# Performance work log

Hardware: AMD Instinct MI355X
Metric: run time of the kernel (lower is better)

## Reference

```python
import jax, jax.numpy as jnp
import numpy as np

# config matching init_kwargs
C = 256; G = 16; GC = C // G; K = 3; P = K * K
PAD = 1; STR = 1; DIL = 1; OFFSET_SCALE = 1.0
N, H, W = 8, 64, 64


def setup_inputs() -> dict:
    key = jax.random.key(0)
    ks = jax.random.split(key, 8)
    def rn(k, shape, sc):
        return jax.random.normal(k, shape, jnp.float32) * sc
    return {
        "x": jax.random.normal(ks[0], (N, H, W, C), jnp.float32),
        "dw_w": rn(ks[1], (C, 1, K, K), 0.1),          # depthwise conv weight (OIHW, groups=C)
        "dw_b": jnp.zeros((C,), jnp.float32),
        "ln_g": jnp.ones((C,), jnp.float32),
        "ln_b": jnp.zeros((C,), jnp.float32),
        "off_w": rn(ks[2], (G * P * 2, C), 0.01),      # offset head (small so offsets stay sane)
        "off_b": jnp.zeros((G * P * 2,), jnp.float32),
        "mask_w": rn(ks[3], (G * P, C), 0.01),
        "mask_b": jnp.zeros((G * P,), jnp.float32),
        "in_w": rn(ks[4], (C, C), 0.05),
        "in_b": jnp.zeros((C,), jnp.float32),
        "out_w": rn(ks[5], (C, C), 0.05),
        "out_b": jnp.zeros((C,), jnp.float32),
    }


def _layer_norm(x, g, b, eps=1e-6):
    m = x.mean(-1, keepdims=True)
    v = ((x - m) ** 2).mean(-1, keepdims=True)
    return (x - m) * jax.lax.rsqrt(v + eps) * g + b


def _grid_sample_bilinear(img, grid):
    # img: (B, Cc, Hh, Ww); grid: (B, L, P, 2) normalized to [-1, 1], (x, y) order.
    # Matches torch.grid_sample(mode='bilinear', padding_mode='zeros', align_corners=False).
    B, Cc, Hh, Ww = img.shape
    gx = (grid[..., 0] + 1.0) * (Ww * 0.5) - 0.5
    gy = (grid[..., 1] + 1.0) * (Hh * 0.5) - 0.5
    x0 = jnp.floor(gx); y0 = jnp.floor(gy)
    tx = gx - x0; ty = gy - y0
    img_f = img.reshape(B, Cc, Hh * Ww)
    def corner(xi, yi, w):
        valid = (xi >= 0) & (xi < Ww) & (yi >= 0) & (yi < Hh)
        idx = (jnp.clip(yi, 0, Hh - 1) * Ww + jnp.clip(xi, 0, Ww - 1)).astype(jnp.int32)
        v = jnp.take_along_axis(img_f, idx.reshape(B, 1, -1), axis=2)  # (B, Cc, L*P)
        return v * (w * valid).reshape(B, 1, -1)
    out = (corner(x0, y0, (1 - tx) * (1 - ty)) + corner(x0 + 1, y0, tx * (1 - ty))
           + corner(x0, y0 + 1, (1 - tx) * ty) + corner(x0 + 1, y0 + 1, tx * ty))
    return out.reshape(B, Cc, grid.shape[1], grid.shape[2])  # (B, Cc, L, P)


def _dcnv3_core(x, offset, mask):
    # x: (N,H,W,C) value features; offset: (N,H,W,G*P*2); mask: (N,H,W,G*P)
    xpad = jnp.pad(x, ((0, 0), (PAD, PAD), (PAD, PAD), (0, 0)))
    Hi, Wi = H + 2 * PAD, W + 2 * PAD
    Ho, Wo = H, W
    # reference points (centers of receptive field), normalized by padded size
    start = (DIL * (K - 1)) // 2 + 0.5
    ry = (start + jnp.arange(Ho, dtype=jnp.float32) * STR) / Hi
    rx = (start + jnp.arange(Wo, dtype=jnp.float32) * STR) / Wi
    ref = jnp.stack([jnp.broadcast_to(rx[None, :], (Ho, Wo)),
                     jnp.broadcast_to(ry[:, None], (Ho, Wo))], -1)  # (Ho,Wo,2) (x,y)
    # dilation grid, x-major flattening to match torch meshgrid('ij') ordering
    d = jnp.arange(K, dtype=jnp.float32) * DIL - (DIL * (K - 1)) // 2
    kgrid = jnp.stack([jnp.repeat(d, K) / Wi, jnp.tile(d, K) / Hi], -1)  # (P,2)
    off = offset.reshape(N, Ho, Wo, G, P, 2)
    norm = jnp.array([Wi, Hi], jnp.float32)
    loc = (ref[None, :, :, None, None, :]
           + kgrid[None, None, None, None, :, :] * OFFSET_SCALE
           + off * OFFSET_SCALE / norm)                      # (N,Ho,Wo,G,P,2)
    sg = (2.0 * loc - 1.0).reshape(N, Ho * Wo, G, P, 2)
    sg = sg.transpose(0, 2, 1, 3, 4).reshape(N * G, Ho * Wo, P, 2)
    val = xpad.reshape(N, Hi * Wi, G * GC).transpose(0, 2, 1).reshape(N * G, GC, Hi, Wi)
    samp = _grid_sample_bilinear(val, sg)                    # (N*G, GC, Ho*Wo, P)
    m = mask.reshape(N, Ho * Wo, G, P).transpose(0, 2, 1, 3).reshape(N * G, 1, Ho * Wo, P)
    out = (samp * m).sum(-1)                                 # (N*G, GC, Ho*Wo)
    return out.reshape(N, G * GC, Ho * Wo).transpose(0, 2, 1).reshape(N, Ho, Wo, C)


def reference(x, dw_w, dw_b, ln_g, ln_b, off_w, off_b, mask_w, mask_b, in_w, in_b, out_w, out_b):
    xp = x @ in_w.T + in_b                                   # input_proj (values)
    # depthwise conv -> LN (channels_last) -> exact GELU
    y = jax.lax.conv_general_dilated(
        x.transpose(0, 3, 1, 2), dw_w, (1, 1), ((PAD, PAD), (PAD, PAD)),
        feature_group_count=C, dimension_numbers=('NCHW', 'OIHW', 'NCHW'))
    y = y + dw_b[None, :, None, None]
    x1 = jax.nn.gelu(_layer_norm(y.transpose(0, 2, 3, 1), ln_g, ln_b), approximate=False)
    offset = x1 @ off_w.T + off_b                            # (N,H,W,G*P*2)
    mlogits = (x1 @ mask_w.T + mask_b).reshape(N, H, W, G, P)
    mask = jax.nn.softmax(mlogits, axis=-1).reshape(N, H, W, G * P)
    out = _dcnv3_core(xp, offset, mask)
    return out @ out_w.T + out_b
```

## Files before the change

### kernel.cpp

```cpp
#include <hip/hip_runtime.h>


#define LL 32768
#define CC 256
#define HSTR 448

typedef __bf16 bf16;
typedef __bf16 bf16x4 __attribute__((ext_vector_type(4)));
typedef __bf16 bf16x8 __attribute__((ext_vector_type(8)));
typedef float f32x4v __attribute__((ext_vector_type(4)));
typedef float f32x2 __attribute__((ext_vector_type(2)));

__device__ __forceinline__ void gload16(const bf16* g, const bf16* lds_base) {
    __builtin_amdgcn_global_load_lds(
        (const __attribute__((address_space(1))) void*)g,
        (__attribute__((address_space(3))) void*)lds_base, 16, 0, 0);
}

__global__ __launch_bounds__(256) void k_prep(
    const float* __restrict__ in_w, const float* __restrict__ off_w,
    const float* __restrict__ mask_w, const float* __restrict__ out_w,
    const float* __restrict__ dw_w, const float* __restrict__ off_b,
    const float* __restrict__ mask_b,
    bf16* __restrict__ in_h, bf16* __restrict__ hw_h,
    bf16* __restrict__ out_h,
    float* __restrict__ dwT, float* __restrict__ hbias) {
    int idx = blockIdx.x * 256 + threadIdx.x;
    if (idx < 60416) {
        const float* s; bf16* hi; int i;
        if (idx < 16384)      { s = in_w;   hi = in_h;          i = idx; }
        else if (idx < 34816) { s = off_w;  hi = hw_h;          i = idx - 16384; }
        else if (idx < 44032) { s = mask_w; hi = hw_h + 73728;  i = idx - 34816; }
        else                  { s = out_w;  hi = out_h;         i = idx - 44032; }
        float4 v = *(const float4*)(s + (size_t)i * 4);
        bf16x4 h;
        h[0] = (bf16)v.x; h[1] = (bf16)v.y; h[2] = (bf16)v.z; h[3] = (bf16)v.w;
        *(bf16x4*)(hi + (size_t)i * 4) = h;
    } else if (idx < 62720) {
        int e = idx - 60416;
        int c = e & 255, j = e >> 8;
        dwT[j * 256 + c] = dw_w[c * 9 + j];
    } else if (idx < 63232) {
        int e = idx - 62720;
        hbias[e] = (e < 288) ? off_b[e] : (e < 432 ? mask_b[e - 288] : 0.f);
    } else if (idx < 68352) {
        int e = idx - 63232;
        bf16x4 z = {(bf16)0.f, (bf16)0.f, (bf16)0.f, (bf16)0.f};
        *(bf16x4*)(hw_h + 110592 + (size_t)e * 4) = z;
    }
}

__global__ __launch_bounds__(256) void k_dwln(
    const float* __restrict__ x, const float* __restrict__ dwT,
    const float* __restrict__ dw_b, const float* __restrict__ ln_g,
    const float* __restrict__ ln_b, bf16* __restrict__ x1h,
    bf16* __restrict__ xb) {
    int t = threadIdx.x;
    int q = t >> 6, u = t & 63;
    int l = blockIdx.x * 4 + q;
    int w = l & 63, h = (l >> 6) & 63, n = l >> 12;
    int c0 = u * 4;

    float4 acc = *(const float4*)(dw_b + c0);
    float4 xc = {0.f, 0.f, 0.f, 0.f};
#pragma unroll
    for (int kh = 0; kh < 3; ++kh) {
        int hh = h + kh - 1;
        if (hh < 0 || hh >= 64) continue;
#pragma unroll
        for (int kw = 0; kw < 3; ++kw) {
            int ww = w + kw - 1;
            if (ww < 0 || ww >= 64) continue;
            float4 xv = *(const float4*)(x + (size_t)(((n * 64 + hh) * 64) + ww) * CC + c0);
            if (kh == 1 && kw == 1) xc = xv;
            float4 wv = *(const float4*)(dwT + (kh * 3 + kw) * 256 + c0);
            acc.x += xv.x * wv.x; acc.y += xv.y * wv.y;
            acc.z += xv.z * wv.z; acc.w += xv.w * wv.w;
        }
    }
    bf16x4 xcb;
    xcb[0] = (bf16)xc.x; xcb[1] = (bf16)xc.y;
    xcb[2] = (bf16)xc.z; xcb[3] = (bf16)xc.w;
    *(bf16x4*)(xb + (size_t)l * CC + c0) = xcb;

    float s = acc.x + acc.y + acc.z + acc.w;
    float ss = acc.x * acc.x + acc.y * acc.y + acc.z * acc.z + acc.w * acc.w;
#pragma unroll
    for (int d = 1; d < 64; d <<= 1) {
        s += __shfl_xor(s, d);
        ss += __shfl_xor(ss, d);
    }
    float mean = s * (1.0f / 256.0f);
    float var = ss * (1.0f / 256.0f) - mean * mean;
    float rstd = rsqrtf(var + 1e-6f);
    float4 gv = *(const float4*)(ln_g + c0);
    float4 bv = *(const float4*)(ln_b + c0);
    float xn0 = (acc.x - mean) * rstd * gv.x + bv.x;
    float xn1 = (acc.y - mean) * rstd * gv.y + bv.y;
    float xn2 = (acc.z - mean) * rstd * gv.z + bv.z;
    float xn3 = (acc.w - mean) * rstd * gv.w + bv.w;
    bf16x4 oh;
    oh[0] = (bf16)(0.5f * xn0 * (1.0f + erff(xn0 * 0.70710678118654752f)));
    oh[1] = (bf16)(0.5f * xn1 * (1.0f + erff(xn1 * 0.70710678118654752f)));
    oh[2] = (bf16)(0.5f * xn2 * (1.0f + erff(xn2 * 0.70710678118654752f)));
    oh[3] = (bf16)(0.5f * xn3 * (1.0f + erff(xn3 * 0.70710678118654752f)));
    *(bf16x4*)(x1h + (size_t)l * CC + c0) = oh;
}

__device__ __forceinline__ void gemm_core(
    const bf16* __restrict__ A, const bf16* __restrict__ Wh,
    const float* __restrict__ bias, bf16* __restrict__ Cbf,
    int Nout, int cstride, int mb, int nb) {
    int t = threadIdx.x, wave = t >> 6, lane = t & 63;
    int wm = wave & 1, wn = wave >> 1;
    int fm = lane & 15, fq = lane >> 4;

    __shared__ bf16 smem[24576];

    const bf16* gbase[4];
    int lofs[4];
#pragma unroll
    for (int j = 0; j < 4; ++j) {
        int seg = wave * 4 + j;
        int arr = seg >> 3;
        int row = (seg & 7) * 16 + (lane >> 2);
        int col = (lane & 3) * 8;
        gbase[j] = (arr == 0) ? (A + (size_t)(mb + row) * CC + col)
                              : (Wh + (size_t)(nb + row) * CC + col);
        lofs[j] = seg * 512;
    }

    f32x4v acc[4][4];
#pragma unroll
    for (int i = 0; i < 4; ++i)
#pragma unroll
        for (int j = 0; j < 4; ++j) acc[i][j] = (f32x4v){0.f, 0.f, 0.f, 0.f};

#pragma unroll
    for (int j = 0; j < 4; ++j) gload16(gbase[j], smem + lofs[j]);
#pragma unroll
    for (int j = 0; j < 4; ++j) gload16(gbase[j] + 32, smem + 8192 + lofs[j]);

#pragma unroll
    for (int kt = 0; kt < 8; ++kt) {
        if (kt < 7)
            asm volatile("s_waitcnt vmcnt(4)\n\ts_barrier" ::: "memory");
        else
            asm volatile("s_waitcnt vmcnt(0)\n\ts_barrier" ::: "memory");
        if (kt < 6) {
#pragma unroll
            for (int j = 0; j < 4; ++j)
                gload16(gbase[j] + (kt + 2) * 32,
                        smem + ((kt + 2) % 3) * 8192 + lofs[j]);
        }
        const bf16* buf = smem + (kt % 3) * 8192;
        bf16x8 af[4], bfh[4];
#pragma unroll
        for (int i = 0; i < 4; ++i)
            af[i] = *(const bf16x8*)&buf[(wm * 64 + i * 16 + fm) * 32 + fq * 8];
#pragma unroll
        for (int j = 0; j < 4; ++j)
            bfh[j] = *(const bf16x8*)&buf[4096 + (wn * 64 + j * 16 + fm) * 32 + fq * 8];
#pragma unroll
        for (int i = 0; i < 4; ++i)
#pragma unroll
            for (int j = 0; j < 4; ++j)
                acc[i][j] = __builtin_amdgcn_mfma_f32_16x16x32_bf16(
                    af[i], bfh[j], acc[i][j], 0, 0, 0);
    }

#pragma unroll
    for (int j = 0; j < 4; ++j) {
        int n_g = nb + wn * 64 + j * 16 + fm;
        if (n_g >= Nout) continue;
        float bv = bias[n_g];
#pragma unroll
        for (int i = 0; i < 4; ++i) {
            int m_g = mb + wm * 64 + i * 16 + fq * 4;
#pragma unroll
            for (int rg = 0; rg < 4; ++rg)
                Cbf[(size_t)(m_g + rg) * cstride + n_g] = (bf16)(acc[i][j][rg] + bv);
        }
    }
}

__global__ __launch_bounds__(256) void k_gemm_ih(
    const bf16* __restrict__ xb, const bf16* __restrict__ x1h,
    const bf16* __restrict__ in_h, const bf16* __restrict__ hw_h,
    const float* __restrict__ in_b, const float* __restrict__ hbias,
    bf16* __restrict__ xpb, bf16* __restrict__ headb) {
    int mb = blockIdx.x * 128;
    int y = blockIdx.y;
    const bf16 *A, *W;
    const float* bs;
    bf16* Cb;
    int Nout, cstride, nb;
    if (y < 2) { A = xb;  W = in_h; bs = in_b;  Cb = xpb;   Nout = 256; cstride = 256;  nb = y * 128; }
    else       { A = x1h; W = hw_h; bs = hbias; Cb = headb; Nout = 432; cstride = HSTR; nb = (y - 2) * 128; }
    gemm_core(A, W, bs, Cb, Nout, cstride, mb, nb);
}

__global__ __launch_bounds__(256) void k_gemm_out(
    const bf16* __restrict__ A, const bf16* __restrict__ Wh,
    const float* __restrict__ bias, float* __restrict__ C32) {
    int mb = blockIdx.x * 64, nb = blockIdx.y * 128;
    int t = threadIdx.x, wave = t >> 6, lane = t & 63;
    int wm = wave & 1, wn = wave >> 1;
    int fm = lane & 15, fq = lane >> 4;

    __shared__ bf16 smem[18432];

    const bf16* gbase[3];
    int lofs[3];
#pragma unroll
    for (int j = 0; j < 3; ++j) {
        int seg = wave * 3 + j;
        int r16 = (seg < 4) ? seg : (seg - 4);
        int row = r16 * 16 + (lane >> 2);
        int col = (lane & 3) * 8;
        gbase[j] = (seg < 4) ? (A + (size_t)(mb + row) * CC + col)
                             : (Wh + (size_t)(nb + row) * CC + col);
        lofs[j] = seg * 512;
    }

    f32x4v acc[2][4];
#pragma unroll
    for (int i = 0; i < 2; ++i)
#pragma unroll
        for (int j = 0; j < 4; ++j) acc[i][j] = (f32x4v){0.f, 0.f, 0.f, 0.f};

#pragma unroll
    for (int j = 0; j < 3; ++j) gload16(gbase[j], smem + lofs[j]);
#pragma unroll
    for (int j = 0; j < 3; ++j) gload16(gbase[j] + 32, smem + 6144 + lofs[j]);

#pragma unroll
    for (int kt = 0; kt < 8; ++kt) {
        if (kt < 7)
            asm volatile("s_waitcnt vmcnt(3)\n\ts_barrier" ::: "memory");
        else
            asm volatile("s_waitcnt vmcnt(0)\n\ts_barrier" ::: "memory");
        if (kt < 6) {
#pragma unroll
            for (int j = 0; j < 3; ++j)
                gload16(gbase[j] + (kt + 2) * 32,
                        smem + ((kt + 2) % 3) * 6144 + lofs[j]);
        }
        const bf16* buf = smem + (kt % 3) * 6144;
        bf16x8 af[2], bfh[4];
#pragma unroll
        for (int i = 0; i < 2; ++i)
            af[i] = *(const bf16x8*)&buf[(wm * 32 + i * 16 + fm) * 32 + fq * 8];
#pragma unroll
        for (int j = 0; j < 4; ++j)
            bfh[j] = *(const bf16x8*)&buf[2048 + (wn * 64 + j * 16 + fm) * 32 + fq * 8];
#pragma unroll
        for (int i = 0; i < 2; ++i)
#pragma unroll
            for (int j = 0; j < 4; ++j)
                acc[i][j] = __builtin_amdgcn_mfma_f32_16x16x32_bf16(
                    af[i], bfh[j], acc[i][j], 0, 0, 0);
    }

#pragma unroll
    for (int j = 0; j < 4; ++j) {
        int n_g = nb + wn * 64 + j * 16 + fm;
        float bv = bias[n_g];
#pragma unroll
        for (int i = 0; i < 2; ++i) {
            int m_g = mb + wm * 32 + i * 16 + fq * 4;
#pragma unroll
            for (int rg = 0; rg < 4; ++rg)
                C32[(size_t)(m_g + rg) * 256 + n_g] = acc[i][j][rg] + bv;
        }
    }
}

__device__ __forceinline__ void mac8(f32x2 acc[4], bf16x8 v, float wt) {
    union { bf16x8 b; unsigned u[4]; } cu;
    cu.b = v;
    f32x2 wv = {wt, wt};
#pragma unroll
    for (int i = 0; i < 4; ++i) {
        f32x2 a;
        a.x = __uint_as_float(cu.u[i] << 16);
        a.y = __uint_as_float(cu.u[i] & 0xffff0000u);
        acc[i] += a * wv;
    }
}

__global__ __launch_bounds__(256) void k_gather(
    const bf16* __restrict__ xp, const bf16* __restrict__ head,
    bf16* __restrict__ rows) {
    int t = threadIdx.x;
    int q = t >> 5, u = t & 31;
    int l = blockIdx.x * 8 + q;
    int w = l & 63, h = (l >> 6) & 63, n = l >> 12;

    __shared__ float CW[8][576];
    __shared__ int BASE[8][144];

    for (int j = u; j < 432; j += 32) CW[q][j] = (float)head[(size_t)l * HSTR + j];
    __syncthreads();

    if (u < 16) {
        int g = u;
        float mx = -1e30f;
#pragma unroll
        for (int p = 0; p < 9; ++p) mx = fmaxf(mx, CW[q][288 + g * 9 + p]);
        float s = 0.f, e[9];
#pragma unroll
        for (int p = 0; p < 9; ++p) { e[p] = expf(CW[q][288 + g * 9 + p] - mx); s += e[p]; }
        float inv = 1.0f / s;
#pragma unroll
        for (int p = 0; p < 9; ++p) CW[q][288 + g * 9 + p] = e[p] * inv;
    }
    __syncthreads();

    float4 cwr[5];
    int baser[5];
#pragma unroll
    for (int k = 0; k < 5; ++k) {
        if (k < 4 || u < 16) {
            int ei = u + 32 * k;
            int g = ei / 9, p = ei - g * 9;
            float ox = CW[q][g * 18 + p * 2 + 0];
            float oy = CW[q][g * 18 + p * 2 + 1];
            float m  = CW[q][288 + ei];
            float ax = (float)(w + (p / 3) - 1) + ox;
            float ay = (float)(h + (p % 3) - 1) + oy;
            float x0f = floorf(ax), y0f = floorf(ay);
            int x0 = (int)x0f, y0 = (int)y0f;
            float tx = ax - x0f, ty = ay - y0f;
            int xb, yb;
            float wxa, wxb, wya, wyb;
            if (x0 < 0)       { xb = 0;  wxa = (x0 == -1) ? tx : 0.f; wxb = 0.f; }
            else if (x0 > 62) { xb = 62; wxa = 0.f; wxb = (x0 == 63) ? (1.f - tx) : 0.f; }
            else              { xb = x0; wxa = 1.f - tx; wxb = tx; }
            if (y0 < 0)       { yb = 0;  wya = (y0 == -1) ? ty : 0.f; wyb = 0.f; }
            else if (y0 > 62) { yb = 62; wya = 0.f; wyb = (y0 == 63) ? (1.f - ty) : 0.f; }
            else              { yb = y0; wya = 1.f - ty; wyb = ty; }
            float4 cw;
            cw.x = m * wxa * wya; cw.y = m * wxb * wya;
            cw.z = m * wxa * wyb; cw.w = m * wxb * wyb;
            cwr[k] = cw;
            baser[k] = (n << 20) + (yb * 64 + xb) * 256;
        }
    }
    __syncthreads();
#pragma unroll
    for (int k = 0; k < 5; ++k) {
        if (k < 4 || u < 16) {
            int ei = u + 32 * k;
            *(float4*)&CW[q][ei * 4] = cwr[k];
            BASE[q][ei] = baser[k];
        }
    }
    __syncthreads();

    int g = u >> 1;
    int c0 = g * 16 + (u & 1) * 8;
    const bf16* xpc = xp + c0;
    f32x2 acc[4];
    acc[0] = (f32x2){0.f, 0.f}; acc[1] = (f32x2){0.f, 0.f};
    acc[2] = (f32x2){0.f, 0.f}; acc[3] = (f32x2){0.f, 0.f};
#pragma unroll
    for (int p = 0; p < 9; ++p) {
        int ei = g * 9 + p;
        float4 cw = *(const float4*)&CW[q][ei * 4];
        int base = BASE[q][ei];
        const bf16* p0 = xpc + base;
        const bf16* p1 = p0 + 16384;
        bf16x8 v00 = *(const bf16x8*)(p0);
        bf16x8 v01 = *(const bf16x8*)(p0 + 256);
        bf16x8 v10 = *(const bf16x8*)(p1);
        bf16x8 v11 = *(const bf16x8*)(p1 + 256);
        mac8(acc, v00, cw.x);
        mac8(acc, v01, cw.y);
        mac8(acc, v10, cw.z);
        mac8(acc, v11, cw.w);
    }
    bf16x8 oh;
    oh[0] = (bf16)acc[0].x; oh[1] = (bf16)acc[0].y;
    oh[2] = (bf16)acc[1].x; oh[3] = (bf16)acc[1].y;
    oh[4] = (bf16)acc[2].x; oh[5] = (bf16)acc[2].y;
    oh[6] = (bf16)acc[3].x; oh[7] = (bf16)acc[3].y;
    *(bf16x8*)(rows + (size_t)l * CC + c0) = oh;
}

__device__ __forceinline__ float dot256f(const float* a, const float* wrow) {
    const float4* w4 = (const float4*)wrow;
    float s = 0.f;
#pragma unroll 16
    for (int i = 0; i < 64; ++i) {
        float4 u = w4[i];
        const float* ap = a + i * 4;
        s += ap[0] * u.x + ap[1] * u.y + ap[2] * u.z + ap[3] * u.w;
    }
    return s;
}

__global__ __launch_bounds__(256) void k_inproj_fb(
    const float* __restrict__ x, const float* __restrict__ in_w,
    const float* __restrict__ in_b, float* __restrict__ xp) {
    int l = blockIdx.x;
    int t = threadIdx.x;
    __shared__ float xa[256];
    xa[t] = x[l * CC + t];
    __syncthreads();
    xp[l * CC + t] = dot256f(xa, in_w + t * CC) + in_b[t];
}

__device__ __forceinline__ float fetch_px_fb(const float* base, int yy, int xx) {
    if (xx < 0 || xx >= 64 || yy < 0 || yy >= 64) return 0.f;
    return base[(yy * 64 + xx) * CC];
}

__global__ __launch_bounds__(256) void k_main_fb(
    const float* __restrict__ x, const float* __restrict__ xp,
    const float* __restrict__ dw_w, const float* __restrict__ dw_b,
    const float* __restrict__ ln_g, const float* __restrict__ ln_b,
    const float* __restrict__ off_w, const float* __restrict__ off_b,
    const float* __restrict__ mask_w, const float* __restrict__ mask_b,
    const float* __restrict__ out_w, const float* __restrict__ out_b,
    float* __restrict__ out) {
    int l = blockIdx.x;
    int t = threadIdx.x;
    int w = l & 63, h = (l >> 6) & 63, n = l >> 12;
    __shared__ float x1[256];
    __shared__ float red[256];
    __shared__ float offs[288];
    __shared__ float ms[144];
    __shared__ float row[256];

    float acc = dw_b[t];
#pragma unroll
    for (int kh = 0; kh < 3; ++kh) {
        int hh = h + kh - 1;
        if (hh < 0 || hh >= 64) continue;
#pragma unroll
        for (int kw = 0; kw < 3; ++kw) {
            int ww = w + kw - 1;
            if (ww < 0 || ww >= 64) continue;
            acc += x[(((n * 64 + hh) * 64) + ww) * CC + t] * dw_w[t * 9 + kh * 3 + kw];
        }
    }
    red[t] = acc;
    __syncthreads();
    for (int s = 128; s > 0; s >>= 1) {
        if (t < s) red[t] += red[t + s];
        __syncthreads();
    }
    float mean = red[0] * (1.0f / 256.0f);
    __syncthreads();
    float d = acc - mean;
    red[t] = d * d;
    __syncthreads();
    for (int s = 128; s > 0; s >>= 1) {
        if (t < s) red[t] += red[t + s];
        __syncthreads();
    }
    float var = red[0] * (1.0f / 256.0f);
    float xn = d * rsqrtf(var + 1e-6f) * ln_g[t] + ln_b[t];
    x1[t] = 0.5f * xn * (1.0f + erff(xn * 0.70710678118654752f));
    __syncthreads();

    offs[t] = dot256f(x1, off_w + t * CC) + off_b[t];
    if (t < 32) {
        int j = 256 + t;
        offs[j] = dot256f(x1, off_w + j * CC) + off_b[j];
    }
    if (t < 144) ms[t] = dot256f(x1, mask_w + t * CC) + mask_b[t];
    __syncthreads();

    if (t < 16) {
        int g = t;
        float mx = -1e30f;
#pragma unroll
        for (int p = 0; p < 9; ++p) mx = fmaxf(mx, ms[g * 9 + p]);
        float s = 0.f, e[9];
#pragma unroll
        for (int p = 0; p < 9; ++p) { e[p] = expf(ms[g * 9 + p] - mx); s += e[p]; }
        float inv = 1.0f / s;
#pragma unroll
        for (int p = 0; p < 9; ++p) ms[g * 9 + p] = e[p] * inv;
    }
    __syncthreads();

    int g = t >> 4;
    const float* base = xp + (size_t)n * 64 * 64 * CC + t;
    float acc2 = 0.f;
#pragma unroll
    for (int p = 0; p < 9; ++p) {
        float ox = offs[g * 18 + p * 2 + 0];
        float oy = offs[g * 18 + p * 2 + 1];
        float ax = (float)(w + (p / 3) - 1) + ox;
        float ay = (float)(h + (p % 3) - 1) + oy;
        float x0f = floorf(ax), y0f = floorf(ay);
        int x0 = (int)x0f, y0 = (int)y0f;
        float tx = ax - x0f, ty = ay - y0f;
        float v00 = fetch_px_fb(base, y0, x0);
        float v01 = fetch_px_fb(base, y0, x0 + 1);
        float v10 = fetch_px_fb(base, y0 + 1, x0);
        float v11 = fetch_px_fb(base, y0 + 1, x0 + 1);
        float bl = (v00 * (1.f - tx) + v01 * tx) * (1.f - ty) +
                   (v10 * (1.f - tx) + v11 * tx) * ty;
        acc2 += ms[g * 9 + p] * bl;
    }
    row[t] = acc2;
    __syncthreads();
    out[l * CC + t] = dot256f(row, out_w + t * CC) + out_b[t];
}

extern "C" void kernel_launch(void* const* d_in, const int* in_sizes, int n_in,
                              void* d_out, int out_size, void* d_ws,
                              size_t ws_size, hipStream_t stream) {
    const float* x      = (const float*)d_in[0];
    const float* dw_w   = (const float*)d_in[1];
    const float* dw_b   = (const float*)d_in[2];
    const float* ln_g   = (const float*)d_in[3];
    const float* ln_b   = (const float*)d_in[4];
    const float* off_w  = (const float*)d_in[5];
    const float* off_b  = (const float*)d_in[6];
    const float* mask_w = (const float*)d_in[7];
    const float* mask_b = (const float*)d_in[8];
    const float* in_w   = (const float*)d_in[9];
    const float* in_b   = (const float*)d_in[10];
    const float* out_w  = (const float*)d_in[11];
    const float* out_b  = (const float*)d_in[12];
    float* out = (float*)d_out;

    const size_t szBF    = (size_t)LL * CC * 2;
    const size_t szHEADB = (size_t)LL * HSTR * 2;
    const size_t szWB    = 1048576;
    const size_t need    = 3 * szBF + szHEADB + szWB;

    dim3 blk(256);
    if (ws_size >= need) {
        char* p = (char*)d_ws;
        bf16* x1h = (bf16*)p; p += szBF;
        bf16* xpb = (bf16*)p; p += szBF;
        bf16* xb  = (bf16*)p; p += szBF;
        bf16* headb = (bf16*)p; p += szHEADB;
        bf16* in_h  = (bf16*)p; p += 131072;
        bf16* hw_h  = (bf16*)p; p += 262144;
        bf16* out_h = (bf16*)p; p += 131072;
        float* dwT  = (float*)p; p += 9216;
        float* hbias = (float*)p;
        bf16* rows = x1h;

        k_prep<<<dim3(267), blk, 0, stream>>>(in_w, off_w, mask_w, out_w, dw_w,
                                              off_b, mask_b, in_h, hw_h, out_h,
                                              dwT, hbias);
        k_dwln<<<dim3(LL / 4), blk, 0, stream>>>(x, dwT, dw_b, ln_g, ln_b, x1h, xb);
        k_gemm_ih<<<dim3(256, 6), blk, 0, stream>>>(
            xb, x1h, in_h, hw_h, in_b, hbias, xpb, headb);
        k_gather<<<dim3(LL / 8), blk, 0, stream>>>(xpb, headb, rows);
        k_gemm_out<<<dim3(512, 2), blk, 0, stream>>>(rows, out_h, out_b, out);
    } else {
        float* xp = (float*)d_ws;
        k_inproj_fb<<<dim3(LL), blk, 0, stream>>>(x, in_w, in_b, xp);
        k_main_fb<<<dim3(LL), blk, 0, stream>>>(x, xp, dw_w, dw_b, ln_g, ln_b,
                                                off_w, off_b, mask_w, mask_b,
                                                out_w, out_b, out);
    }
}
```

Measured before the change: 196.8 us.

## Fuse weight-prep kernel into depthwise-LN kernel and vectorize gather head loads

Merges the weight conversion/prep kernel into the depthwise conv + LayerNorm kernel as extra blocks, removing one launch. Each dwln block now transposes the depthwise weights into shared memory itself instead of reading a pre-transposed global buffer. The gather kernel loads the head row with 16-byte bf16x8 vector loads instead of scalar loads. The trade-off is redundant per-block weight transposition using integer division, plus an extra barrier in every dwln block.

```diff
diff --git a/kernel.cpp b/kernel.cpp
--- a/kernel.cpp
+++ b/kernel.cpp
@@ -17,47 +17,56 @@
         (__attribute__((address_space(3))) void*)lds_base, 16, 0, 0);
 }
 
-__global__ __launch_bounds__(256) void k_prep(
+__global__ __launch_bounds__(256) void k_dwp(
+    const float* __restrict__ x, const float* __restrict__ dw_w,
+    const float* __restrict__ dw_b, const float* __restrict__ ln_g,
+    const float* __restrict__ ln_b, bf16* __restrict__ x1h,
+    bf16* __restrict__ xb,
     const float* __restrict__ in_w, const float* __restrict__ off_w,
     const float* __restrict__ mask_w, const float* __restrict__ out_w,
-    const float* __restrict__ dw_w, const float* __restrict__ off_b,
-    const float* __restrict__ mask_b,
+    const float* __restrict__ off_b, const float* __restrict__ mask_b,
     bf16* __restrict__ in_h, bf16* __restrict__ hw_h,
-    bf16* __restrict__ out_h,
-    float* __restrict__ dwT, float* __restrict__ hbias) {
-    int idx = blockIdx.x * 256 + threadIdx.x;
-    if (idx < 60416) {
-        const float* s; bf16* hi; int i;
-        if (idx < 16384)      { s = in_w;   hi = in_h;          i = idx; }
-        else if (idx < 34816) { s = off_w;  hi = hw_h;          i = idx - 16384; }
-        else if (idx < 44032) { s = mask_w; hi = hw_h + 73728;  i = idx - 34816; }
-        else                  { s = out_w;  hi = out_h;         i = idx - 44032; }
-        float4 v = *(const float4*)(s + (size_t)i * 4);
-        bf16x4 h;
-        h[0] = (bf16)v.x; h[1] = (bf16)v.y; h[2] = (bf16)v.z; h[3] = (bf16)v.w;
-        *(bf16x4*)(hi + (size_t)i * 4) = h;
-    } else if (idx < 62720) {
-        int e = idx - 60416;
-        int c = e & 255, j = e >> 8;
-        dwT[j * 256 + c] = dw_w[c * 9 + j];
-    } else if (idx < 63232) {
-        int e = idx - 62720;
-        hbias[e] = (e < 288) ? off_b[e] : (e < 432 ? mask_b[e - 288] : 0.f);
-    } else if (idx < 68352) {
-        int e = idx - 63232;
-        bf16x4 z = {(bf16)0.f, (bf16)0.f, (bf16)0.f, (bf16)0.f};
-        *(bf16x4*)(hw_h + 110592 + (size_t)e * 4) = z;
-    }
-}
-
-__global__ __launch_bounds__(256) void k_dwln(
-    const float* __restrict__ x, const float* __restrict__ dwT,
-    const float* __restrict__ dw_b, const float* __restrict__ ln_g,
-    const float* __restrict__ ln_b, bf16* __restrict__ x1h,
-    bf16* __restrict__ xb) {
+    bf16* __restrict__ out_h, float* __restrict__ hbias) {
     int t = threadIdx.x;
+    int b = blockIdx.x;
+    if (b >= 8192) {
+        int idx = (b - 8192) * 256 + t;
+        if (idx < 60416) {
+            const float* s; bf16* hi; int i;
+            if (idx < 16384)      { s = in_w;   hi = in_h;          i = idx; }
+            else if (idx < 34816) { s = off_w;  hi = hw_h;          i = idx - 16384; }
+            else if (idx < 44032) { s = mask_w; hi = hw_h + 73728;  i = idx - 34816; }
+            else                  { s = out_w;  hi = out_h;         i = idx - 44032; }
+            float4 v = *(const float4*)(s + (size_t)i * 4);
+            bf16x4 hh;
+            hh[0] = (bf16)v.x; hh[1] = (bf16)v.y; hh[2] = (bf16)v.z; hh[3] = (bf16)v.w;
+            *(bf16x4*)(hi + (size_t)i * 4) = hh;
+        } else if (idx < 60928) {
+            int e = idx - 60416;
+            hbias[e] = (e < 288) ? off_b[e] : (e < 432 ? mask_b[e - 288] : 0.f);
+        } else if (idx < 66048) {
+            int e = idx - 60928;
+            bf16x4 z = {(bf16)0.f, (bf16)0.f, (bf16)0.f, (bf16)0.f};
+            *(bf16x4*)(hw_h + 110592 + (size_t)e * 4) = z;
+        }
+        return;
+    }
+    __shared__ float wlds[2304];
+    for (int i4 = t; i4 < 576; i4 += 256) {
+        float4 v = *(const float4*)(dw_w + i4 * 4);
+        int e = i4 * 4;
+#pragma unroll
+        for (int k = 0; k < 4; ++k) {
+            int ee = e + k;
+            int c = ee / 9;
+            int j = ee - c * 9;
+            wlds[j * 256 + c] = v[k];
+        }
+    }
+    __syncthreads();
+
     int q = t >> 6, u = t & 63;
-    int l = blockIdx.x * 4 + q;
+    int l = b * 4 + q;
     int w = l & 63, h = (l >> 6) & 63, n = l >> 12;
     int c0 = u * 4;
 
@@ -73,7 +82,7 @@
             if (ww < 0 || ww >= 64) continue;
             float4 xv = *(const float4*)(x + (size_t)(((n * 64 + hh) * 64) + ww) * CC + c0);
             if (kh == 1 && kw == 1) xc = xv;
-            float4 wv = *(const float4*)(dwT + (kh * 3 + kw) * 256 + c0);
+            float4 wv = *(const float4*)&wlds[(kh * 3 + kw) * 256 + c0];
             acc.x += xv.x * wv.x; acc.y += xv.y * wv.y;
             acc.z += xv.z * wv.z; acc.w += xv.w * wv.w;
         }
@@ -300,7 +309,18 @@
     __shared__ float CW[8][576];
     __shared__ int BASE[8][144];
 
-    for (int j = u; j < 432; j += 32) CW[q][j] = (float)head[(size_t)l * HSTR + j];
+#pragma unroll
+    for (int k = 0; k < 2; ++k) {
+        int cj = u + 27 * k;
+        if (u < 27) {
+            bf16x8 v = *(const bf16x8*)(head + (size_t)l * HSTR + cj * 8);
+            float4 f0, f1;
+            f0.x = (float)v[0]; f0.y = (float)v[1]; f0.z = (float)v[2]; f0.w = (float)v[3];
+            f1.x = (float)v[4]; f1.y = (float)v[5]; f1.z = (float)v[6]; f1.w = (float)v[7];
+            *(float4*)&CW[q][cj * 8] = f0;
+            *(float4*)&CW[q][cj * 8 + 4] = f1;
+        }
+    }
     __syncthreads();
 
     if (u < 16) {
@@ -545,14 +565,13 @@
         bf16* in_h  = (bf16*)p; p += 131072;
         bf16* hw_h  = (bf16*)p; p += 262144;
         bf16* out_h = (bf16*)p; p += 131072;
-        float* dwT  = (float*)p; p += 9216;
         float* hbias = (float*)p;
         bf16* rows = x1h;
 
-        k_prep<<<dim3(267), blk, 0, stream>>>(in_w, off_w, mask_w, out_w, dw_w,
-                                              off_b, mask_b, in_h, hw_h, out_h,
-                                              dwT, hbias);
-        k_dwln<<<dim3(LL / 4), blk, 0, stream>>>(x, dwT, dw_b, ln_g, ln_b, x1h, xb);
+        k_dwp<<<dim3(8450), blk, 0, stream>>>(
+            x, dw_w, dw_b, ln_g, ln_b, x1h, xb,
+            in_w, off_w, mask_w, out_w, off_b, mask_b,
+            in_h, hw_h, out_h, hbias);
         k_gemm_ih<<<dim3(256, 6), blk, 0, stream>>>(
             xb, x1h, in_h, hw_h, in_b, hbias, xpb, headb);
         k_gather<<<dim3(LL / 8), blk, 0, stream>>>(xpb, headb, rows);
```

Result: faster. 190.2 us (-3.3%).
